# Kernel optimization log

Hardware: AMD Instinct MI355X
Metric: run time of the kernel (lower is better)

The kernel has to match this reference:

```python
import jax, jax.numpy as jnp
import numpy as np

N_PATIENT = 50000
N_GENE = 20000
N_EDGE = 640000
P_DIM, G_DIM, H, OUT = 64, 32, 128, 8


def setup_inputs() -> dict:
    key = jax.random.key(0)
    ks = jax.random.split(key, 20)
    s = 0.02
    return {
        "x_patient": jax.random.normal(ks[0], (N_PATIENT, P_DIM), jnp.float32),
        "x_gene": jax.random.normal(ks[1], (N_GENE, G_DIM), jnp.float32),
        "edge_index": jax.random.randint(ks[2], (2, N_EDGE), 0, N_GENE, jnp.int32),
        # patient MLP
        "W_p1": jax.random.normal(ks[3], (P_DIM, H), jnp.float32) * s,
        "b_p1": jnp.zeros((H,), jnp.float32),
        "W_p2": jax.random.normal(ks[4], (H, H), jnp.float32) * s,
        "b_p2": jnp.zeros((H,), jnp.float32),
        # gene MLP
        "W_g1": jax.random.normal(ks[5], (G_DIM, H), jnp.float32) * s,
        "b_g1": jnp.zeros((H,), jnp.float32),
        "W_g2": jax.random.normal(ks[6], (H, H), jnp.float32) * s,
        "b_g2": jnp.zeros((H,), jnp.float32),
        # SAGEConv 1: lin_l acts on aggregated src, lin_r (root) on dst
        "W1_l": jax.random.normal(ks[7], (H, H), jnp.float32) * s,
        "b1_l": jnp.zeros((H,), jnp.float32),
        "W1_r": jax.random.normal(ks[8], (H, H), jnp.float32) * s,
        # SAGEConv 2
        "W2_l": jax.random.normal(ks[9], (H, H), jnp.float32) * s,
        "b2_l": jnp.zeros((H,), jnp.float32),
        "W2_r": jax.random.normal(ks[10], (H, H), jnp.float32) * s,
        # final fc
        "W_fc": jax.random.normal(ks[11], (H, OUT), jnp.float32) * s,
        "b_fc": jnp.zeros((OUT,), jnp.float32),
    }


def reference(x_patient, x_gene, edge_index,
              W_p1, b_p1, W_p2, b_p2,
              W_g1, b_g1, W_g2, b_g2,
              W1_l, b1_l, W1_r,
              W2_l, b2_l, W2_r,
              W_fc, b_fc):
    # node-type MLPs
    p = jax.nn.relu(x_patient @ W_p1 + b_p1) @ W_p2 + b_p2   # [N_P, H]
    g = jax.nn.relu(x_gene @ W_g1 + b_g1) @ W_g2 + b_g2       # [N_G, H]

    src, dst = edge_index[0], edge_index[1]
    # gene_x is unchanged between layers, so the sum-aggregate is identical
    # for both SAGEConv layers: compute the gather + segment-sum once.
    agg = jax.ops.segment_sum(g[src], dst, num_segments=x_patient.shape[0])  # [N_P, H]

    # SAGEConv(aggr='sum'): out = lin_l(agg) + lin_r(x_dst), bias in lin_l
    p = jax.nn.relu(agg @ W1_l + b1_l + p @ W1_r)
    p = jax.nn.relu(agg @ W2_l + b2_l + p @ W2_r)
    return p @ W_fc + b_fc  # [N_P, OUT]
```

## Files before the change

### kernel.cpp

```cpp
#include <hip/hip_runtime.h>

#define NP 50000
#define NG 20000
#define NE 640000
#define PD 64
#define GD 32
#define HD 128
#define OD 8
#define CAP 96

using f32x4 = __attribute__((ext_vector_type(4))) float;
using s16x8 = __attribute__((ext_vector_type(8))) short;

__device__ __forceinline__ unsigned short f2bf(float f) {
    union { float f; unsigned u; } v; v.f = f;
    const unsigned r = v.u + 0x7FFFu + ((v.u >> 16) & 1u);
    return (unsigned short)(r >> 16);
}
__device__ __forceinline__ float bfpair_lo(unsigned v) {
    union { unsigned u; float f; } x; x.u = v << 16; return x.f;
}
__device__ __forceinline__ float bfpair_hi(unsigned v) {
    union { unsigned u; float f; } x; x.u = v & 0xFFFF0000u; return x.f;
}

#define TOT_SWZ 112640
#define TOT_UNITS (TOT_SWZ + NP / 4)

__global__ __launch_bounds__(256) void swz_kernel(
    const float* __restrict__ Wp1, const float* __restrict__ Wp2,
    const float* __restrict__ W1l, const float* __restrict__ W1r,
    const float* __restrict__ W2l, const float* __restrict__ W2r,
    const float* __restrict__ Wfc,
    const float* __restrict__ Wg1, const float* __restrict__ Wg2,
    unsigned short* __restrict__ wswz, int* __restrict__ cursor)
{
    const int u = blockIdx.x * 256 + threadIdx.x;
    if (u < TOT_SWZ) {
        const float* src; int K, Nr, doff;
        if      (u <   8192) { src = Wp1; K =  64; Nr = HD; doff = 0; }
        else if (u <  24576) { src = Wp2; K = 128; Nr = HD; doff = 8192; }
        else if (u <  40960) { src = W1l; K = 128; Nr = HD; doff = 24576; }
        else if (u <  57344) { src = W1r; K = 128; Nr = HD; doff = 40960; }
        else if (u <  73728) { src = W2l; K = 128; Nr = HD; doff = 57344; }
        else if (u <  90112) { src = W2r; K = 128; Nr = HD; doff = 73728; }
        else if (u <  92160) { src = Wfc; K = 128; Nr = OD; doff = 90112; }
        else if (u <  96256) { src = Wg1; K =  32; Nr = HD; doff = 92160; }
        else                 { src = Wg2; K = 128; Nr = HD; doff = 96256; }
        const int e  = u - doff;
        const int j  = e & 7;
        const int ln = (e >> 3) & 63;
        const int f  = e >> 9;
        const int KC = K >> 5;
        const int c  = f % KC;
        const int n0 = f / KC;
        const int k  = c * 32 + (ln >> 4) * 8 + j;
        const int n  = n0 * 16 + (ln & 15);
        wswz[u] = f2bf((n < Nr) ? src[k * Nr + n] : 0.f);
    } else if (u < TOT_UNITS) {
        const int i = u - TOT_SWZ;
        *(int4*)&cursor[i * 4] = (int4){0, 0, 0, 0};
    }
}

#define GENE_TILES 313
#define FILL_BLOCKS ((NE + 255) / 256)

__global__ __launch_bounds__(256) void genefill_kernel(
    const float* __restrict__ xg,
    const unsigned short* __restrict__ wswz,
    const float* __restrict__ bg1, const float* __restrict__ bg2,
    unsigned short* __restrict__ g,
    const int* __restrict__ ei, int* __restrict__ cursor, int* __restrict__ pad)
{
    __shared__ unsigned short lds[4][16 * 136];
    if (blockIdx.x >= GENE_TILES) {
        const int e = (blockIdx.x - GENE_TILES) * 256 + threadIdx.x;
        if (e < NE) {
            const int s = ei[e];
            const int d = ei[NE + e];
            const int pos = atomicAdd(&cursor[d], 1);
            if (pos < CAP) pad[d * CAP + pos] = s;
        }
        return;
    }
    const unsigned short* wg1 = wswz + 92160;
    const unsigned short* wg2 = wswz + 96256;

    const int lane = threadIdx.x & 63;
    const int wid  = threadIdx.x >> 6;
    const int quad = lane >> 4;
    const int l16  = lane & 15;
    const int row0 = blockIdx.x * 64 + wid * 16;
    const int arow = min(row0 + l16, NG - 1);
    unsigned short* X = lds[wid];
    const f32x4 Z = {0.f, 0.f, 0.f, 0.f};

    s16x8 a;
    {
        const float* xr = xg + (size_t)arow * GD + quad * 8;
        const f32x4 u0 = *(const f32x4*)xr;
        const f32x4 u1 = *(const f32x4*)(xr + 4);
#pragma unroll
        for (int j = 0; j < 4; ++j) {
            a[j]     = (short)f2bf(u0[j]);
            a[4 + j] = (short)f2bf(u1[j]);
        }
    }
    f32x4 C[8];
#pragma unroll
    for (int n = 0; n < 8; ++n) {
        const s16x8 b = *(const s16x8*)&wg1[(n * 64 + lane) * 8];
        C[n] = __builtin_amdgcn_mfma_f32_16x16x32_bf16(a, b, Z, 0, 0, 0);
    }
#pragma unroll
    for (int n = 0; n < 8; ++n) {
        const float bias = bg1[n * 16 + l16];
#pragma unroll
        for (int r = 0; r < 4; ++r)
            X[(quad * 4 + r) * 136 + n * 16 + l16] = f2bf(fmaxf(C[n][r] + bias, 0.f));
    }
    s16x8 pa[4];
#pragma unroll
    for (int c = 0; c < 4; ++c) pa[c] = *(const s16x8*)&X[l16 * 136 + c * 32 + quad * 8];
#pragma unroll
    for (int n = 0; n < 8; ++n) {
        C[n] = Z;
#pragma unroll
        for (int c = 0; c < 4; ++c) {
            const s16x8 b = *(const s16x8*)&wg2[((n * 4 + c) * 64 + lane) * 8];
            C[n] = __builtin_amdgcn_mfma_f32_16x16x32_bf16(pa[c], b, C[n], 0, 0, 0);
        }
    }
#pragma unroll
    for (int n = 0; n < 8; ++n) {
        const float bias = bg2[n * 16 + l16];
#pragma unroll
        for (int r = 0; r < 4; ++r) {
            const int row = row0 + quad * 4 + r;
            if (row < NG) g[(size_t)row * HD + n * 16 + l16] = f2bf(C[n][r] + bias);
        }
    }
}

__global__ __launch_bounds__(256) void agg_kernel(
    const int* __restrict__ cursor, const int* __restrict__ pad,
    const unsigned short* __restrict__ g, unsigned short* __restrict__ aggb)
{
    const int row  = __builtin_amdgcn_readfirstlane(blockIdx.x * 4 + (threadIdx.x >> 6));
    const int lane = threadIdx.x & 63;
    const int grp  = lane >> 4;
    const int sub  = lane & 15;
    const int cnt  = min(cursor[row], CAP);
    const int rb   = row * CAP;

    float acc0[8] = {0.f, 0.f, 0.f, 0.f, 0.f, 0.f, 0.f, 0.f};
    float acc1[8] = {0.f, 0.f, 0.f, 0.f, 0.f, 0.f, 0.f, 0.f};
    if (cnt > 0) {
        int4 q0 = *(const int4*)&pad[rb];
        int4 q1 = (cnt > 4) ? *(const int4*)&pad[rb + 4] : q0;
        for (int i = 0; i < cnt; i += 8) {
            const int4 c0 = q0;
            const int4 c1 = q1;
            if (i + 8  < cnt) q0 = *(const int4*)&pad[rb + i + 8];
            if (i + 12 < cnt) q1 = *(const int4*)&pad[rb + i + 12];
            int r0 = (grp == 0) ? c0.x : (grp == 1) ? c0.y : (grp == 2) ? c0.z : c0.w;
            int r1 = (grp == 0) ? c1.x : (grp == 1) ? c1.y : (grp == 2) ? c1.z : c1.w;
            const bool v0 = (i + grp) < cnt;
            const bool v1 = (i + 4 + grp) < cnt;
            r0 = v0 ? r0 : c0.x;
            r1 = v1 ? r1 : c0.x;
            const float s0 = v0 ? 1.f : 0.f;
            const float s1 = v1 ? 1.f : 0.f;
            const s16x8 g0 = *(const s16x8*)&g[(size_t)r0 * HD + sub * 8];
            const s16x8 g1 = *(const s16x8*)&g[(size_t)r1 * HD + sub * 8];
            const unsigned* d0 = (const unsigned*)&g0;
            const unsigned* d1 = (const unsigned*)&g1;
#pragma unroll
            for (int k = 0; k < 4; ++k) {
                acc0[2 * k]     = fmaf(bfpair_lo(d0[k]), s0, acc0[2 * k]);
                acc0[2 * k + 1] = fmaf(bfpair_hi(d0[k]), s0, acc0[2 * k + 1]);
                acc1[2 * k]     = fmaf(bfpair_lo(d1[k]), s1, acc1[2 * k]);
                acc1[2 * k + 1] = fmaf(bfpair_hi(d1[k]), s1, acc1[2 * k + 1]);
            }
        }
#pragma unroll
        for (int k = 0; k < 8; ++k) {
            acc0[k] += acc1[k];
            acc0[k] += __shfl_xor(acc0[k], 16);
            acc0[k] += __shfl_xor(acc0[k], 32);
        }
    }
    if (lane < 16) {
        unsigned o[4];
#pragma unroll
        for (int k = 0; k < 4; ++k)
            o[k] = (unsigned)f2bf(acc0[2 * k]) | ((unsigned)f2bf(acc0[2 * k + 1]) << 16);
        *(int4*)&aggb[(size_t)row * HD + lane * 8] = *(int4*)o;
    }
}

__global__ __launch_bounds__(256) void patient_kernel(
    const float* __restrict__ xp, const unsigned short* __restrict__ aggb,
    const unsigned short* __restrict__ wswz,
    const float* __restrict__ bp1, const float* __restrict__ bp2,
    const float* __restrict__ b1l, const float* __restrict__ b2l,
    const float* __restrict__ bfc,
    float* __restrict__ out)
{
    const unsigned short* wp1 = wswz + 0;
    const unsigned short* wp2 = wswz + 8192;
    const unsigned short* w1l = wswz + 24576;
    const unsigned short* w1r = wswz + 40960;
    const unsigned short* w2l = wswz + 57344;
    const unsigned short* w2r = wswz + 73728;
    const unsigned short* wfc = wswz + 90112;

    __shared__ unsigned short lds[4][32 * 136];
    const int lane = threadIdx.x & 63;
    const int wid  = threadIdx.x >> 6;
    const int quad = lane >> 4;
    const int l16  = lane & 15;
    const int row0 = blockIdx.x * 128 + wid * 32;
    const int rA = min(row0 + l16, NP - 1);
    const int rB = min(row0 + 16 + l16, NP - 1);
    unsigned short* X = lds[wid];
    const f32x4 Z = {0.f, 0.f, 0.f, 0.f};

    f32x4 CA[8], CB[8];
    {
        s16x8 aA0, aA1, aB0, aB1;
        {
            const float* xa = xp + (size_t)rA * PD + quad * 8;
            const float* xb = xp + (size_t)rB * PD + quad * 8;
            const f32x4 uA0 = *(const f32x4*)xa;
            const f32x4 uA1 = *(const f32x4*)(xa + 4);
            const f32x4 uA2 = *(const f32x4*)(xa + 32);
            const f32x4 uA3 = *(const f32x4*)(xa + 36);
            const f32x4 uB0 = *(const f32x4*)xb;
            const f32x4 uB1 = *(const f32x4*)(xb + 4);
            const f32x4 uB2 = *(const f32x4*)(xb + 32);
            const f32x4 uB3 = *(const f32x4*)(xb + 36);
#pragma unroll
            for (int j = 0; j < 4; ++j) {
                aA0[j]     = (short)f2bf(uA0[j]);
                aA0[4 + j] = (short)f2bf(uA1[j]);
                aA1[j]     = (short)f2bf(uA2[j]);
                aA1[4 + j] = (short)f2bf(uA3[j]);
                aB0[j]     = (short)f2bf(uB0[j]);
                aB0[4 + j] = (short)f2bf(uB1[j]);
                aB1[j]     = (short)f2bf(uB2[j]);
                aB1[4 + j] = (short)f2bf(uB3[j]);
            }
        }
#pragma unroll
        for (int n = 0; n < 8; ++n) {
            const s16x8 b0 = *(const s16x8*)&wp1[((n * 2 + 0) * 64 + lane) * 8];
            const s16x8 b1 = *(const s16x8*)&wp1[((n * 2 + 1) * 64 + lane) * 8];
            CA[n] = __builtin_amdgcn_mfma_f32_16x16x32_bf16(aA0, b0, Z, 0, 0, 0);
            CA[n] = __builtin_amdgcn_mfma_f32_16x16x32_bf16(aA1, b1, CA[n], 0, 0, 0);
            CB[n] = __builtin_amdgcn_mfma_f32_16x16x32_bf16(aB0, b0, Z, 0, 0, 0);
            CB[n] = __builtin_amdgcn_mfma_f32_16x16x32_bf16(aB1, b1, CB[n], 0, 0, 0);
        }
    }
#pragma unroll
    for (int n = 0; n < 8; ++n) {
        const float bias = bp1[n * 16 + l16];
#pragma unroll
        for (int r = 0; r < 4; ++r) {
            X[(quad * 4 + r) * 136 + n * 16 + l16]      = f2bf(fmaxf(CA[n][r] + bias, 0.f));
            X[(16 + quad * 4 + r) * 136 + n * 16 + l16] = f2bf(fmaxf(CB[n][r] + bias, 0.f));
        }
    }
    {
        s16x8 pA[4], pB[4];
#pragma unroll
        for (int c = 0; c < 4; ++c) {
            pA[c] = *(const s16x8*)&X[l16 * 136 + c * 32 + quad * 8];
            pB[c] = *(const s16x8*)&X[(16 + l16) * 136 + c * 32 + quad * 8];
        }
#pragma unroll
        for (int n = 0; n < 8; ++n) {
            CA[n] = Z; CB[n] = Z;
#pragma unroll
            for (int c = 0; c < 4; ++c) {
                const s16x8 b = *(const s16x8*)&wp2[((n * 4 + c) * 64 + lane) * 8];
                CA[n] = __builtin_amdgcn_mfma_f32_16x16x32_bf16(pA[c], b, CA[n], 0, 0, 0);
                CB[n] = __builtin_amdgcn_mfma_f32_16x16x32_bf16(pB[c], b, CB[n], 0, 0, 0);
            }
        }
#pragma unroll
        for (int n = 0; n < 8; ++n) {
            const float bias = bp2[n * 16 + l16];
#pragma unroll
            for (int r = 0; r < 4; ++r) {
                X[(quad * 4 + r) * 136 + n * 16 + l16]      = f2bf(CA[n][r] + bias);
                X[(16 + quad * 4 + r) * 136 + n * 16 + l16] = f2bf(CB[n][r] + bias);
            }
        }
    }
    {
        s16x8 pA[4], pB[4], agA[4], agB[4];
#pragma unroll
        for (int c = 0; c < 4; ++c) {
            pA[c]  = *(const s16x8*)&X[l16 * 136 + c * 32 + quad * 8];
            pB[c]  = *(const s16x8*)&X[(16 + l16) * 136 + c * 32 + quad * 8];
            agA[c] = *(const s16x8*)&aggb[(size_t)rA * HD + c * 32 + quad * 8];
            agB[c] = *(const s16x8*)&aggb[(size_t)rB * HD + c * 32 + quad * 8];
        }
#pragma unroll
        for (int n = 0; n < 8; ++n) {
            CA[n] = Z; CB[n] = Z;
#pragma unroll
            for (int c = 0; c < 4; ++c) {
                const s16x8 bl = *(const s16x8*)&w1l[((n * 4 + c) * 64 + lane) * 8];
                const s16x8 br = *(const s16x8*)&w1r[((n * 4 + c) * 64 + lane) * 8];
                CA[n] = __builtin_amdgcn_mfma_f32_16x16x32_bf16(agA[c], bl, CA[n], 0, 0, 0);
                CA[n] = __builtin_amdgcn_mfma_f32_16x16x32_bf16(pA[c],  br, CA[n], 0, 0, 0);
                CB[n] = __builtin_amdgcn_mfma_f32_16x16x32_bf16(agB[c], bl, CB[n], 0, 0, 0);
                CB[n] = __builtin_amdgcn_mfma_f32_16x16x32_bf16(pB[c],  br, CB[n], 0, 0, 0);
            }
        }
#pragma unroll
        for (int n = 0; n < 8; ++n) {
            const float bias = b1l[n * 16 + l16];
#pragma unroll
            for (int r = 0; r < 4; ++r) {
                X[(quad * 4 + r) * 136 + n * 16 + l16]      = f2bf(fmaxf(CA[n][r] + bias, 0.f));
                X[(16 + quad * 4 + r) * 136 + n * 16 + l16] = f2bf(fmaxf(CB[n][r] + bias, 0.f));
            }
        }
    }
    {
        s16x8 hA[4], hB[4], agA[4], agB[4];
#pragma unroll
        for (int c = 0; c < 4; ++c) {
            hA[c]  = *(const s16x8*)&X[l16 * 136 + c * 32 + quad * 8];
            hB[c]  = *(const s16x8*)&X[(16 + l16) * 136 + c * 32 + quad * 8];
            agA[c] = *(const s16x8*)&aggb[(size_t)rA * HD + c * 32 + quad * 8];
            agB[c] = *(const s16x8*)&aggb[(size_t)rB * HD + c * 32 + quad * 8];
        }
#pragma unroll
        for (int n = 0; n < 8; ++n) {
            CA[n] = Z; CB[n] = Z;
#pragma unroll
            for (int c = 0; c < 4; ++c) {
                const s16x8 bl = *(const s16x8*)&w2l[((n * 4 + c) * 64 + lane) * 8];
                const s16x8 br = *(const s16x8*)&w2r[((n * 4 + c) * 64 + lane) * 8];
                CA[n] = __builtin_amdgcn_mfma_f32_16x16x32_bf16(agA[c], bl, CA[n], 0, 0, 0);
                CA[n] = __builtin_amdgcn_mfma_f32_16x16x32_bf16(hA[c],  br, CA[n], 0, 0, 0);
                CB[n] = __builtin_amdgcn_mfma_f32_16x16x32_bf16(agB[c], bl, CB[n], 0, 0, 0);
                CB[n] = __builtin_amdgcn_mfma_f32_16x16x32_bf16(hB[c],  br, CB[n], 0, 0, 0);
            }
        }
#pragma unroll
        for (int n = 0; n < 8; ++n) {
            const float bias = b2l[n * 16 + l16];
#pragma unroll
            for (int r = 0; r < 4; ++r) {
                X[(quad * 4 + r) * 136 + n * 16 + l16]      = f2bf(fmaxf(CA[n][r] + bias, 0.f));
                X[(16 + quad * 4 + r) * 136 + n * 16 + l16] = f2bf(fmaxf(CB[n][r] + bias, 0.f));
            }
        }
    }
    {
        s16x8 hA[4], hB[4];
#pragma unroll
        for (int c = 0; c < 4; ++c) {
            hA[c] = *(const s16x8*)&X[l16 * 136 + c * 32 + quad * 8];
            hB[c] = *(const s16x8*)&X[(16 + l16) * 136 + c * 32 + quad * 8];
        }
        f32x4 CoA = Z, CoB = Z;
#pragma unroll
        for (int c = 0; c < 4; ++c) {
            const s16x8 b = *(const s16x8*)&wfc[(c * 64 + lane) * 8];
            CoA = __builtin_amdgcn_mfma_f32_16x16x32_bf16(hA[c], b, CoA, 0, 0, 0);
            CoB = __builtin_amdgcn_mfma_f32_16x16x32_bf16(hB[c], b, CoB, 0, 0, 0);
        }
        if (l16 < OD) {
            const float bias = bfc[l16];
#pragma unroll
            for (int r = 0; r < 4; ++r) {
                const int rowA = row0 + quad * 4 + r;
                const int rowB = row0 + 16 + quad * 4 + r;
                if (rowA < NP) out[(size_t)rowA * OD + l16] = CoA[r] + bias;
                if (rowB < NP) out[(size_t)rowB * OD + l16] = CoB[r] + bias;
            }
        }
    }
}

extern "C" void kernel_launch(void* const* d_in, const int* in_sizes, int n_in,
                              void* d_out, int out_size, void* d_ws, size_t ws_size,
                              hipStream_t stream)
{
    const float* xp  = (const float*)d_in[0];
    const float* xg  = (const float*)d_in[1];
    const int*   ei  = (const int*)d_in[2];
    const float* Wp1 = (const float*)d_in[3];
    const float* bp1 = (const float*)d_in[4];
    const float* Wp2 = (const float*)d_in[5];
    const float* bp2 = (const float*)d_in[6];
    const float* Wg1 = (const float*)d_in[7];
    const float* bg1 = (const float*)d_in[8];
    const float* Wg2 = (const float*)d_in[9];
    const float* bg2 = (const float*)d_in[10];
    const float* W1l = (const float*)d_in[11];
    const float* b1l = (const float*)d_in[12];
    const float* W1r = (const float*)d_in[13];
    const float* W2l = (const float*)d_in[14];
    const float* b2l = (const float*)d_in[15];
    const float* W2r = (const float*)d_in[16];
    const float* Wfc = (const float*)d_in[17];
    const float* bfc = (const float*)d_in[18];
    float* out = (float*)d_out;

    char* ws = (char*)d_ws;
    unsigned short* g_b   = (unsigned short*)(ws + 0);
    unsigned short* wswz  = (unsigned short*)(ws + 5120000);
    int*            cursor= (int*)(ws + 5345280);
    int*            pad   = (int*)(ws + 5545280);
    unsigned short* agg_b = (unsigned short*)(ws + 13225280);

    swz_kernel<<<(TOT_UNITS + 255) / 256, 256, 0, stream>>>(
        Wp1, Wp2, W1l, W1r, W2l, W2r, Wfc, Wg1, Wg2, wswz, cursor);

    genefill_kernel<<<GENE_TILES + FILL_BLOCKS, 256, 0, stream>>>(
        xg, wswz, bg1, bg2, g_b, ei, cursor, pad);

    agg_kernel<<<NP / 4, 256, 0, stream>>>(cursor, pad, g_b, agg_b);

    patient_kernel<<<(NP + 127) / 128, 256, 0, stream>>>(
        xp, agg_b, wswz, bp1, bp2, b1l, b2l, bfc, out);
}
```

Baseline: 189.4 us.

## Split per-destination edge buckets into four sub-buckets to cut atomic contention

The CSR-like fill now spreads each destination's edges over four sub-buckets chosen by edge index. Each has its own atomic cursor, so atomic conflicts on hot destinations drop. The aggregation kernel gives each 16-lane group one sub-bucket and unrolls the gather four edges at a time, then reduces across groups with shuffles. The trade-off is per-group loop trip counts that now differ within a wave, and edges being dropped if any sub-bucket exceeds 32 entries, which is unlikely for these random inputs.

```diff
diff --git a/kernel.cpp b/kernel.cpp
--- a/kernel.cpp
+++ b/kernel.cpp
@@ -7,7 +7,9 @@
 #define GD 32
 #define HD 128
 #define OD 8
-#define CAP 96
+#define NSUB 4
+#define SUBCAP 32
+#define ROWCAP (NSUB * SUBCAP)
 
 using f32x4 = __attribute__((ext_vector_type(4))) float;
 using s16x8 = __attribute__((ext_vector_type(8))) short;
@@ -25,7 +27,8 @@
 }
 
 #define TOT_SWZ 112640
-#define TOT_UNITS (TOT_SWZ + NP / 4)
+#define CUR_INT4 (NG * NSUB / 4)
+#define TOT_UNITS (TOT_SWZ + CUR_INT4)
 
 __global__ __launch_bounds__(256) void swz_kernel(
     const float* __restrict__ Wp1, const float* __restrict__ Wp2,
@@ -79,8 +82,9 @@
         if (e < NE) {
             const int s = ei[e];
             const int d = ei[NE + e];
-            const int pos = atomicAdd(&cursor[d], 1);
-            if (pos < CAP) pad[d * CAP + pos] = s;
+            const int sub = e & (NSUB - 1);
+            const int pos = atomicAdd(&cursor[d * NSUB + sub], 1);
+            if (pos < SUBCAP) pad[d * ROWCAP + sub * SUBCAP + pos] = s;
         }
         return;
     }
@@ -147,55 +151,50 @@
     const int* __restrict__ cursor, const int* __restrict__ pad,
     const unsigned short* __restrict__ g, unsigned short* __restrict__ aggb)
 {
-    const int row  = __builtin_amdgcn_readfirstlane(blockIdx.x * 4 + (threadIdx.x >> 6));
+    const int row  = blockIdx.x * 4 + (threadIdx.x >> 6);
     const int lane = threadIdx.x & 63;
     const int grp  = lane >> 4;
     const int sub  = lane & 15;
-    const int cnt  = min(cursor[row], CAP);
-    const int rb   = row * CAP;
-
-    float acc0[8] = {0.f, 0.f, 0.f, 0.f, 0.f, 0.f, 0.f, 0.f};
-    float acc1[8] = {0.f, 0.f, 0.f, 0.f, 0.f, 0.f, 0.f, 0.f};
-    if (cnt > 0) {
-        int4 q0 = *(const int4*)&pad[rb];
-        int4 q1 = (cnt > 4) ? *(const int4*)&pad[rb + 4] : q0;
-        for (int i = 0; i < cnt; i += 8) {
-            const int4 c0 = q0;
-            const int4 c1 = q1;
-            if (i + 8  < cnt) q0 = *(const int4*)&pad[rb + i + 8];
-            if (i + 12 < cnt) q1 = *(const int4*)&pad[rb + i + 12];
-            int r0 = (grp == 0) ? c0.x : (grp == 1) ? c0.y : (grp == 2) ? c0.z : c0.w;
-            int r1 = (grp == 0) ? c1.x : (grp == 1) ? c1.y : (grp == 2) ? c1.z : c1.w;
-            const bool v0 = (i + grp) < cnt;
-            const bool v1 = (i + 4 + grp) < cnt;
-            r0 = v0 ? r0 : c0.x;
-            r1 = v1 ? r1 : c0.x;
-            const float s0 = v0 ? 1.f : 0.f;
-            const float s1 = v1 ? 1.f : 0.f;
-            const s16x8 g0 = *(const s16x8*)&g[(size_t)r0 * HD + sub * 8];
-            const s16x8 g1 = *(const s16x8*)&g[(size_t)r1 * HD + sub * 8];
-            const unsigned* d0 = (const unsigned*)&g0;
-            const unsigned* d1 = (const unsigned*)&g1;
-#pragma unroll
-            for (int k = 0; k < 4; ++k) {
-                acc0[2 * k]     = fmaf(bfpair_lo(d0[k]), s0, acc0[2 * k]);
-                acc0[2 * k + 1] = fmaf(bfpair_hi(d0[k]), s0, acc0[2 * k + 1]);
-                acc1[2 * k]     = fmaf(bfpair_lo(d1[k]), s1, acc1[2 * k]);
-                acc1[2 * k + 1] = fmaf(bfpair_hi(d1[k]), s1, acc1[2 * k + 1]);
-            }
-        }
-#pragma unroll
-        for (int k = 0; k < 8; ++k) {
-            acc0[k] += acc1[k];
-            acc0[k] += __shfl_xor(acc0[k], 16);
-            acc0[k] += __shfl_xor(acc0[k], 32);
-        }
+
+    float acc[8] = {0.f, 0.f, 0.f, 0.f, 0.f, 0.f, 0.f, 0.f};
+    const int cnt = (row < NG) ? min(cursor[row * NSUB + grp], SUBCAP) : 0;
+    const int base = row * ROWCAP + grp * SUBCAP;
+    for (int i = 0; i < cnt; i += 4) {
+        const int4 q = *(const int4*)&pad[base + i];
+        int r0 = q.x, r1 = q.y, r2 = q.z, r3 = q.w;
+        const bool v1 = (i + 1) < cnt, v2 = (i + 2) < cnt, v3 = (i + 3) < cnt;
+        r1 = v1 ? r1 : q.x;  r2 = v2 ? r2 : q.x;  r3 = v3 ? r3 : q.x;
+        const float s1 = v1 ? 1.f : 0.f, s2 = v2 ? 1.f : 0.f, s3 = v3 ? 1.f : 0.f;
+        const s16x8 g0 = *(const s16x8*)&g[(size_t)r0 * HD + sub * 8];
+        const s16x8 g1 = *(const s16x8*)&g[(size_t)r1 * HD + sub * 8];
+        const s16x8 g2 = *(const s16x8*)&g[(size_t)r2 * HD + sub * 8];
+        const s16x8 g3 = *(const s16x8*)&g[(size_t)r3 * HD + sub * 8];
+        const unsigned* d0 = (const unsigned*)&g0;
+        const unsigned* d1 = (const unsigned*)&g1;
+        const unsigned* d2 = (const unsigned*)&g2;
+        const unsigned* d3 = (const unsigned*)&g3;
+#pragma unroll
+        for (int k = 0; k < 4; ++k) {
+            acc[2 * k]     += bfpair_lo(d0[k]);
+            acc[2 * k + 1] += bfpair_hi(d0[k]);
+            acc[2 * k]     = fmaf(bfpair_lo(d1[k]), s1, acc[2 * k]);
+            acc[2 * k + 1] = fmaf(bfpair_hi(d1[k]), s1, acc[2 * k + 1]);
+            acc[2 * k]     = fmaf(bfpair_lo(d2[k]), s2, acc[2 * k]);
+            acc[2 * k + 1] = fmaf(bfpair_hi(d2[k]), s2, acc[2 * k + 1]);
+            acc[2 * k]     = fmaf(bfpair_lo(d3[k]), s3, acc[2 * k]);
+            acc[2 * k + 1] = fmaf(bfpair_hi(d3[k]), s3, acc[2 * k + 1]);
+        }
+    }
+#pragma unroll
+    for (int k = 0; k < 8; ++k) {
+        acc[k] += __shfl_xor(acc[k], 16);
+        acc[k] += __shfl_xor(acc[k], 32);
     }
     if (lane < 16) {
         unsigned o[4];
 #pragma unroll
         for (int k = 0; k < 4; ++k)
-            o[k] = (unsigned)f2bf(acc0[2 * k]) | ((unsigned)f2bf(acc0[2 * k + 1]) << 16);
+            o[k] = (unsigned)f2bf(acc[2 * k]) | ((unsigned)f2bf(acc[2 * k + 1]) << 16);
         *(int4*)&aggb[(size_t)row * HD + lane * 8] = *(int4*)o;
     }
 }
@@ -419,8 +418,8 @@
     unsigned short* g_b   = (unsigned short*)(ws + 0);
     unsigned short* wswz  = (unsigned short*)(ws + 5120000);
     int*            cursor= (int*)(ws + 5345280);
-    int*            pad   = (int*)(ws + 5545280);
-    unsigned short* agg_b = (unsigned short*)(ws + 13225280);
+    int*            pad   = (int*)(ws + 5665280);
+    unsigned short* agg_b = (unsigned short*)(ws + 15905280);
 
     swz_kernel<<<(TOT_UNITS + 255) / 256, 256, 0, stream>>>(
         Wp1, Wp2, W1l, W1r, W2l, W2r, Wfc, Wg1, Wg2, wswz, cursor);
```

Result: slower. 193.3 us (+2.1%).
